# Kernel optimization log

Hardware: AMD Instinct MI355X
Metric: run time of the kernel (lower is better)

## Reference

```python
import jax, jax.numpy as jnp
import numpy as np

N, H, S, R, T = 32768, 512, 8, 64, 12

def setup_inputs() -> dict:
    key = jax.random.key(0)
    ks = jax.random.split(key, 7)
    scale = 1.0 / np.sqrt(H)
    return {
        "encodings": jax.random.normal(ks[0], (N, H), dtype=jnp.float32),
        "domain_encs": jax.random.normal(ks[1], (S, H), dtype=jnp.float32),
        "Us": jax.random.normal(ks[2], (S, H, R), dtype=jnp.float32) * scale,
        "W1": jax.random.normal(ks[3], (S, H, H), dtype=jnp.float32) * scale,
        "b1": jax.random.normal(ks[4], (S, H), dtype=jnp.float32) * 0.01,
        "W2": jax.random.normal(ks[5], (S, H, T), dtype=jnp.float32) * scale,
        "b2": jax.random.normal(ks[6], (S, T), dtype=jnp.float32) * 0.01,
    }

def reference(encodings, domain_encs, Us, W1, b1, W2, b2):
    # Mahalanobis soft routing. Original computes (p-mu) @ (U U^T) @ (p-mu)^T
    # and takes sqrt(diag) -- algebraically identical to project-then-square-sum.
    diff = encodings[None, :, :] - domain_encs[:, None, :]        # [S, N, H]
    proj = jnp.einsum('snh,shr->snr', diff, Us)                   # [S, N, R]
    dist = jnp.sqrt(jnp.sum(proj * proj, axis=-1))                # [S, N]
    alphas = jax.nn.softmax(-dist, axis=0)                        # softmax over sources

    # Per-source classifier: Dropout(eval=identity) -> ReLU -> Linear(H,H)
    # -> Dropout -> ReLU -> Linear(H,T) -> Sigmoid
    h0 = jax.nn.relu(encodings)                                   # [N, H]
    h1 = jax.nn.relu(jnp.einsum('nh,shk->snk', h0, W1) + b1[:, None, :])  # [S, N, H]
    out = jax.nn.sigmoid(jnp.einsum('snk,skt->snt', h1, W2) + b2[:, None, :])  # [S, N, T]

    # Softmax-weighted combine of expert outputs
    return jnp.sum(alphas[:, :, None] * out, axis=0)              # [N, T]
```

## Files before the change

kernel.cpp:

```cpp
#include <hip/hip_runtime.h>
#include <hip/hip_bf16.h>

typedef unsigned short u16;
typedef __bf16 bf16x8 __attribute__((ext_vector_type(8)));
typedef float f32x4 __attribute__((ext_vector_type(4)));

#define NROWS 32768
#define H 512
#define NS 8
#define NR 64
#define NT 12

#define WS_W1T   0
#define WS_UCT   4194304
#define WS_W2T   4718592
#define WS_CVEC  4849664
#define WS_DIST  4851712

union BFU { __bf16 h; u16 u; };
__device__ __forceinline__ u16 f2bf(float v) { BFU b; b.h = (__bf16)v; return b.u; }

__device__ __forceinline__ void gload16(const u16* g, u16* l) {
  __builtin_amdgcn_global_load_lds(
      (const __attribute__((address_space(1))) unsigned int*)g,
      (__attribute__((address_space(3))) unsigned int*)l, 16, 0, 0);
}

__global__ __launch_bounds__(256) void prep(
    const float* __restrict__ W1, u16* __restrict__ W1T,
    const float* __restrict__ Us, u16* __restrict__ UcatT,
    const float* __restrict__ W2, u16* __restrict__ W2T,
    const float* __restrict__ mu, float* __restrict__ cvec) {
  __shared__ float tile[32][33];
  const int bid = blockIdx.x;
  const int tx = threadIdx.x, ty = threadIdx.y;
  if (bid < 2432) {
    const float* in; u16* out; int Rr, Cc, Cpad, b, r0, c0;
    if (bid < 2048) {
      in = W1; out = W1T; Rr = 512; Cc = 512; Cpad = 512;
      r0 = (bid & 15) * 32; c0 = ((bid >> 4) & 15) * 32; b = bid >> 8;
    } else if (bid < 2304) {
      int t2 = bid - 2048; in = Us; out = UcatT; Rr = 512; Cc = 64; Cpad = 64;
      r0 = (t2 & 15) * 32; c0 = ((t2 >> 4) & 1) * 32; b = t2 >> 5;
    } else {
      int t2 = bid - 2304; in = W2; out = W2T; Rr = 512; Cc = 12; Cpad = 16;
      r0 = (t2 & 15) * 32; c0 = 0; b = t2 >> 4;
    }
#pragma unroll
    for (int i = 0; i < 4; i++) {
      int r = r0 + ty + i * 8, c = c0 + tx;
      float v = 0.f;
      if (r < Rr && c < Cc) v = in[((size_t)b * Rr + r) * Cc + c];
      tile[ty + i * 8][tx] = v;
    }
    __syncthreads();
#pragma unroll
    for (int i = 0; i < 4; i++) {
      int c = c0 + ty + i * 8, r = r0 + tx;
      if (c < Cpad && r < Rr) out[((size_t)b * Cpad + c) * Rr + r] = f2bf(tile[tx][ty + i * 8]);
    }
  } else {
    const int tid = ty * 32 + tx;
    const int idx = (bid - 2432) * 4 + (tid >> 6);
    const int s = idx >> 6, r = idx & 63, t = tid & 63;
    float acc = 0.f;
#pragma unroll
    for (int k = t; k < H; k += 64) acc += mu[s * H + k] * Us[((size_t)s * H + k) * NR + r];
#pragma unroll
    for (int m = 32; m; m >>= 1) acc += __shfl_xor(acc, m, 64);
    if (t == 0) cvec[idx] = acc;
  }
}

__device__ __forceinline__ void stageW16(const u16* __restrict__ g, u16* l, int tid) {
#pragma unroll
  for (int i = 0; i < 4; i++) {
    int flat = tid + i * 256;
    int r = flat >> 5, u = flat & 31;
    gload16(g + (size_t)r * 512 + (u ^ (r & 7)) * 8, l + flat * 8);
  }
}

__device__ __forceinline__ const u16* rchunk(const u16* U, int rcol0, int q) {
  return U + ((size_t)(rcol0 + (q >> 2) * 64 + ((q >> 1) & 1) * 32)) * 512 + (q & 1) * 256;
}

__global__ __launch_bounds__(256, 2) void routing(
    const float* __restrict__ enc, const u16* __restrict__ UcatT,
    const float* __restrict__ cvec, float* __restrict__ distT) {
  __shared__ __align__(16) u16 Wst[3][32 * 256];
  __shared__ float cvS[256];

  const int tid = threadIdx.x;
  const int wave = tid >> 6, lane = tid & 63;
  const int lnm = lane & 15, lnq = lane >> 4;
  const int rb = blockIdx.x >> 1, sg = blockIdx.x & 1;
  const int row0 = rb * 128, sbase = sg * 4;
  const int rcol0 = sbase * 64;

  cvS[tid] = cvec[rcol0 + tid];

  bf16x8 efrag[2][16];
#pragma unroll
  for (int t = 0; t < 2; t++) {
    const float* rp = enc + (size_t)(row0 + wave * 32 + t * 16 + lnm) * H + lnq * 8;
#pragma unroll
    for (int ks = 0; ks < 16; ks++) {
      float4 x0 = *(const float4*)(rp + ks * 32);
      float4 x1 = *(const float4*)(rp + ks * 32 + 4);
      bf16x8 a;
      a[0] = (__bf16)x0.x; a[1] = (__bf16)x0.y; a[2] = (__bf16)x0.z; a[3] = (__bf16)x0.w;
      a[4] = (__bf16)x1.x; a[5] = (__bf16)x1.y; a[6] = (__bf16)x1.z; a[7] = (__bf16)x1.w;
      efrag[t][ks] = a;
    }
  }

  __syncthreads();

  stageW16(rchunk(UcatT, rcol0, 0), Wst[0], tid);
  int cb = 0;
  f32x4 acc[2][2];
#pragma unroll 1
  for (int j = 0; j < 4; j++) {
    float dsq[2] = {0.f, 0.f};
#pragma unroll 1
    for (int wc = 0; wc < 2; wc++) {
#pragma unroll
      for (int t = 0; t < 2; t++) { acc[t][0] = (f32x4){0,0,0,0}; acc[t][1] = (f32x4){0,0,0,0}; }
#pragma unroll
      for (int kh = 0; kh < 2; kh++) {
        const int q = j * 4 + wc * 2 + kh;
        const int nb = (cb == 2) ? 0 : cb + 1;
        if (q + 1 < 16) {
          stageW16(rchunk(UcatT, rcol0, q + 1), Wst[nb], tid);
          asm volatile("s_waitcnt vmcnt(4)" ::: "memory");
        } else {
          asm volatile("s_waitcnt vmcnt(0)" ::: "memory");
        }
        __builtin_amdgcn_s_barrier();
        const u16* buf = Wst[cb];
#pragma unroll
        for (int ks = 0; ks < 8; ks++) {
          const int uu = ((ks * 4 + lnq) ^ (lnm & 7)) * 8;
          bf16x8 w0 = *(const bf16x8*)&buf[lnm * 256 + uu];
          bf16x8 w1 = *(const bf16x8*)&buf[(16 + lnm) * 256 + uu];
#pragma unroll
          for (int t = 0; t < 2; t++) {
            acc[t][0] = __builtin_amdgcn_mfma_f32_16x16x32_bf16(w0, efrag[t][kh * 8 + ks], acc[t][0], 0, 0, 0);
            acc[t][1] = __builtin_amdgcn_mfma_f32_16x16x32_bf16(w1, efrag[t][kh * 8 + ks], acc[t][1], 0, 0, 0);
          }
        }
        cb = nb;
      }
#pragma unroll
      for (int ct = 0; ct < 2; ct++) {
        float4 cv4 = *(const float4*)&cvS[j * 64 + wc * 32 + ct * 16 + lnq * 4];
#pragma unroll
        for (int t = 0; t < 2; t++) {
          float d0 = acc[t][ct][0] - cv4.x, d1 = acc[t][ct][1] - cv4.y;
          float d2 = acc[t][ct][2] - cv4.z, d3 = acc[t][ct][3] - cv4.w;
          dsq[t] += d0 * d0 + d1 * d1 + d2 * d2 + d3 * d3;
        }
      }
    }
#pragma unroll
    for (int t = 0; t < 2; t++) {
      dsq[t] += __shfl_xor(dsq[t], 16, 64);
      dsq[t] += __shfl_xor(dsq[t], 32, 64);
    }
    if (lnq == 0) {
#pragma unroll
      for (int t = 0; t < 2; t++)
        distT[(size_t)(sbase + j) * NROWS + row0 + wave * 32 + t * 16 + lnm] = sqrtf(dsq[t]);
    }
  }
}

#define H1STR 40

__device__ __forceinline__ const u16* chunk_base(const u16* W1g, int q) {
  return W1g + ((size_t)(q >> 5) * 512 + ((q >> 1) & 15) * 32) * 512 + (q & 1) * 256;
}

__global__ __launch_bounds__(256, 2) void moe_main(
    const float* __restrict__ enc, const u16* __restrict__ W1T,
    const u16* __restrict__ W2T, const float* __restrict__ distT,
    const float* __restrict__ b1g, const float* __restrict__ b2g,
    float* __restrict__ out) {
  __shared__ __align__(16) u16 Wst[3][32 * 256];
  __shared__ __align__(16) u16 h1c[128 * H1STR];
  __shared__ float alphS[4][128];

  const int tid = threadIdx.x;
  const int wave = tid >> 6, lane = tid & 63;
  const int lnm = lane & 15, lnq = lane >> 4;
  const int rb = blockIdx.x >> 1, sg = blockIdx.x & 1;
  const int row0 = rb * 128, sbase = sg * 4;

  if (tid < 128) {
    float dv[NS], e[NS];
#pragma unroll
    for (int s2 = 0; s2 < NS; s2++) dv[s2] = distT[(size_t)s2 * NROWS + row0 + tid];
    float dmin = dv[0];
#pragma unroll
    for (int s2 = 1; s2 < NS; s2++) dmin = fminf(dmin, dv[s2]);
    float den = 0.f;
#pragma unroll
    for (int s2 = 0; s2 < NS; s2++) { e[s2] = __expf(dmin - dv[s2]); den += e[s2]; }
    float inv = 1.f / den;
#pragma unroll
    for (int jj = 0; jj < 4; jj++) alphS[jj][tid] = e[sbase + jj] * inv;
  }

  float b2v[4];
#pragma unroll
  for (int j = 0; j < 4; j++) b2v[j] = (lnm < NT) ? b2g[(sbase + j) * NT + lnm] : 0.f;

  bf16x8 efrag[2][16];
#pragma unroll
  for (int t = 0; t < 2; t++) {
    const float* rp = enc + (size_t)(row0 + wave * 32 + t * 16 + lnm) * H + lnq * 8;
#pragma unroll
    for (int ks = 0; ks < 16; ks++) {
      float4 x0 = *(const float4*)(rp + ks * 32);
      float4 x1 = *(const float4*)(rp + ks * 32 + 4);
      bf16x8 a;
      a[0] = (__bf16)fmaxf(x0.x, 0.f); a[1] = (__bf16)fmaxf(x0.y, 0.f);
      a[2] = (__bf16)fmaxf(x0.z, 0.f); a[3] = (__bf16)fmaxf(x0.w, 0.f);
      a[4] = (__bf16)fmaxf(x1.x, 0.f); a[5] = (__bf16)fmaxf(x1.y, 0.f);
      a[6] = (__bf16)fmaxf(x1.z, 0.f); a[7] = (__bf16)fmaxf(x1.w, 0.f);
      efrag[t][ks] = a;
    }
  }

  __syncthreads();

  const u16* W1g = W1T + (size_t)sbase * 512 * 512;
  stageW16(chunk_base(W1g, 0), Wst[0], tid);
  int cb = 0;
  f32x4 acc[2][2];
  float fin[2][4] = {};
#pragma unroll 1
  for (int j = 0; j < 4; j++) {
    const int s = sbase + j;
    f32x4 oacc[2] = {};
#pragma unroll 1
    for (int wc = 0; wc < 16; wc++) {
      const int q = j * 32 + wc * 2;
      float4 bq0 = *(const float4*)&b1g[s * H + wc * 32 + lnq * 4];
      float4 bq1 = *(const float4*)&b1g[s * H + wc * 32 + 16 + lnq * 4];
      bf16x8 bw = *(const bf16x8*)&W2T[((size_t)s * 16 + lnm) * H + wc * 32 + lnq * 8];
      asm volatile("" ::: "memory");
      {
        const int nb = (cb == 2) ? 0 : cb + 1;
        stageW16(chunk_base(W1g, q + 1), Wst[nb], tid);
        asm volatile("s_waitcnt vmcnt(7)" ::: "memory");
        __builtin_amdgcn_s_barrier();
        const u16* buf = Wst[cb];
#pragma unroll
        for (int t = 0; t < 2; t++) {
          acc[t][0] = (f32x4){bq0.x, bq0.y, bq0.z, bq0.w};
          acc[t][1] = (f32x4){bq1.x, bq1.y, bq1.z, bq1.w};
        }
#pragma unroll
        for (int ks = 0; ks < 8; ks++) {
          const int uu = ((ks * 4 + lnq) ^ (lnm & 7)) * 8;
          bf16x8 w0 = *(const bf16x8*)&buf[lnm * 256 + uu];
          bf16x8 w1 = *(const bf16x8*)&buf[(16 + lnm) * 256 + uu];
#pragma unroll
          for (int t = 0; t < 2; t++) {
            acc[t][0] = __builtin_amdgcn_mfma_f32_16x16x32_bf16(w0, efrag[t][ks], acc[t][0], 0, 0, 0);
            acc[t][1] = __builtin_amdgcn_mfma_f32_16x16x32_bf16(w1, efrag[t][ks], acc[t][1], 0, 0, 0);
          }
        }
        cb = nb;
      }
      {
        const int nb = (cb == 2) ? 0 : cb + 1;
        if (q + 2 < 128) {
          stageW16(chunk_base(W1g, q + 2), Wst[nb], tid);
          asm volatile("s_waitcnt vmcnt(4)" ::: "memory");
        } else {
          asm volatile("s_waitcnt vmcnt(0)" ::: "memory");
        }
        __builtin_amdgcn_s_barrier();
        const u16* buf = Wst[cb];
#pragma unroll
        for (int ks = 0; ks < 8; ks++) {
          const int uu = ((ks * 4 + lnq) ^ (lnm & 7)) * 8;
          bf16x8 w0 = *(const bf16x8*)&buf[lnm * 256 + uu];
          bf16x8 w1 = *(const bf16x8*)&buf[(16 + lnm) * 256 + uu];
#pragma unroll
          for (int t = 0; t < 2; t++) {
            acc[t][0] = __builtin_amdgcn_mfma_f32_16x16x32_bf16(w0, efrag[t][8 + ks], acc[t][0], 0, 0, 0);
            acc[t][1] = __builtin_amdgcn_mfma_f32_16x16x32_bf16(w1, efrag[t][8 + ks], acc[t][1], 0, 0, 0);
          }
        }
        cb = nb;
      }
#pragma unroll
      for (int ct = 0; ct < 2; ct++) {
#pragma unroll
        for (int t = 0; t < 2; t++) {
          union { u16 u[4]; uint2 v; } pk;
          pk.u[0] = f2bf(fmaxf(acc[t][ct][0], 0.f));
          pk.u[1] = f2bf(fmaxf(acc[t][ct][1], 0.f));
          pk.u[2] = f2bf(fmaxf(acc[t][ct][2], 0.f));
          pk.u[3] = f2bf(fmaxf(acc[t][ct][3], 0.f));
          *(uint2*)&h1c[(wave * 32 + t * 16 + lnm) * H1STR + ct * 16 + lnq * 4] = pk.v;
        }
      }
      {
#pragma unroll
        for (int t = 0; t < 2; t++) {
          bf16x8 a2 = *(const bf16x8*)&h1c[(wave * 32 + t * 16 + lnm) * H1STR + lnq * 8];
          oacc[t] = __builtin_amdgcn_mfma_f32_16x16x32_bf16(a2, bw, oacc[t], 0, 0, 0);
        }
      }
    }
    {
#pragma unroll
      for (int t = 0; t < 2; t++) {
#pragma unroll
        for (int g = 0; g < 4; g++) {
          float sig = 1.f / (1.f + __expf(-(oacc[t][g] + b2v[j])));
          fin[t][g] += alphS[j][wave * 32 + t * 16 + lnq * 4 + g] * sig;
        }
      }
    }
  }
  if (lnm < NT) {
#pragma unroll
    for (int t = 0; t < 2; t++) {
#pragma unroll
      for (int g = 0; g < 4; g++) {
        int rg = row0 + wave * 32 + t * 16 + lnq * 4 + g;
        atomicAdd(&out[(size_t)rg * NT + lnm], fin[t][g]);
      }
    }
  }
}

extern "C" void kernel_launch(void* const* d_in, const int* in_sizes, int n_in,
                              void* d_out, int out_size, void* d_ws, size_t ws_size,
                              hipStream_t stream) {
  const float* enc = (const float*)d_in[0];
  const float* mu  = (const float*)d_in[1];
  const float* Us  = (const float*)d_in[2];
  const float* W1  = (const float*)d_in[3];
  const float* b1  = (const float*)d_in[4];
  const float* W2  = (const float*)d_in[5];
  const float* b2  = (const float*)d_in[6];
  float* out = (float*)d_out;
  char* ws = (char*)d_ws;
  u16* W1T    = (u16*)(ws + WS_W1T);
  u16* UcatT  = (u16*)(ws + WS_UCT);
  u16* W2T    = (u16*)(ws + WS_W2T);
  float* cvec = (float*)(ws + WS_CVEC);
  float* distT = (float*)(ws + WS_DIST);

  prep<<<2560, dim3(32, 8, 1), 0, stream>>>(W1, W1T, Us, UcatT, W2, W2T, mu, cvec);
  routing<<<512, 256, 0, stream>>>(enc, UcatT, cvec, distT);
  hipMemsetAsync(out, 0, (size_t)out_size * sizeof(float), stream);
  moe_main<<<512, 256, 0, stream>>>(enc, W1T, W2T, distT, b1, b2, out);
}
```

Baseline: 268.3 us.

## Overlap W1 transpose and output zeroing with routing kernel blocks

The large W1 transpose-to-bf16 moves out of the prep kernel into extra blocks of the routing kernel, so it runs alongside the routing GEMM instead of before it. The output memset is replaced by zeroing blocks in that same launch, which removes a separate API call. The aim is to cut serialized launches and let the memory-bound transpose share the GPU with the compute-bound routing work. The cost is that routing_w1 now carries the routing kernel's shared memory footprint and launch bounds for the transpose blocks too, which may limit how many of them fit at once.

```diff
diff --git a/kernel.cpp b/kernel.cpp
--- a/kernel.cpp
+++ b/kernel.cpp
@@ -26,42 +26,38 @@
       (__attribute__((address_space(3))) unsigned int*)l, 16, 0, 0);
 }
 
-__global__ __launch_bounds__(256) void prep(
-    const float* __restrict__ W1, u16* __restrict__ W1T,
+__device__ __forceinline__ void tile_transpose(const float* __restrict__ in,
+    u16* __restrict__ out, int Rr, int Cc, int Cpad, int b, int r0, int c0, int tid) {
+  __shared__ float tile[32][33];
+  const int tx = tid & 31, ty = tid >> 5;
+#pragma unroll
+  for (int i = 0; i < 4; i++) {
+    int r = r0 + ty + i * 8, c = c0 + tx;
+    float v = 0.f;
+    if (r < Rr && c < Cc) v = in[((size_t)b * Rr + r) * Cc + c];
+    tile[ty + i * 8][tx] = v;
+  }
+  __syncthreads();
+#pragma unroll
+  for (int i = 0; i < 4; i++) {
+    int c = c0 + ty + i * 8, r = r0 + tx;
+    if (c < Cpad && r < Rr) out[((size_t)b * Cpad + c) * Rr + r] = f2bf(tile[tx][ty + i * 8]);
+  }
+}
+
+__global__ __launch_bounds__(256) void prepA(
     const float* __restrict__ Us, u16* __restrict__ UcatT,
     const float* __restrict__ W2, u16* __restrict__ W2T,
     const float* __restrict__ mu, float* __restrict__ cvec) {
-  __shared__ float tile[32][33];
-  const int bid = blockIdx.x;
-  const int tx = threadIdx.x, ty = threadIdx.y;
-  if (bid < 2432) {
-    const float* in; u16* out; int Rr, Cc, Cpad, b, r0, c0;
-    if (bid < 2048) {
-      in = W1; out = W1T; Rr = 512; Cc = 512; Cpad = 512;
-      r0 = (bid & 15) * 32; c0 = ((bid >> 4) & 15) * 32; b = bid >> 8;
-    } else if (bid < 2304) {
-      int t2 = bid - 2048; in = Us; out = UcatT; Rr = 512; Cc = 64; Cpad = 64;
-      r0 = (t2 & 15) * 32; c0 = ((t2 >> 4) & 1) * 32; b = t2 >> 5;
-    } else {
-      int t2 = bid - 2304; in = W2; out = W2T; Rr = 512; Cc = 12; Cpad = 16;
-      r0 = (t2 & 15) * 32; c0 = 0; b = t2 >> 4;
-    }
-#pragma unroll
-    for (int i = 0; i < 4; i++) {
-      int r = r0 + ty + i * 8, c = c0 + tx;
-      float v = 0.f;
-      if (r < Rr && c < Cc) v = in[((size_t)b * Rr + r) * Cc + c];
-      tile[ty + i * 8][tx] = v;
-    }
-    __syncthreads();
-#pragma unroll
-    for (int i = 0; i < 4; i++) {
-      int c = c0 + ty + i * 8, r = r0 + tx;
-      if (c < Cpad && r < Rr) out[((size_t)b * Cpad + c) * Rr + r] = f2bf(tile[tx][ty + i * 8]);
-    }
+  const int bid = blockIdx.x, tid = threadIdx.x;
+  if (bid < 256) {
+    tile_transpose(Us, UcatT, 512, 64, 64, bid >> 5, (bid & 15) * 32,
+                   ((bid >> 4) & 1) * 32, tid);
+  } else if (bid < 384) {
+    int t2 = bid - 256;
+    tile_transpose(W2, W2T, 512, 12, 16, t2 >> 4, (t2 & 15) * 32, 0, tid);
   } else {
-    const int tid = ty * 32 + tx;
-    const int idx = (bid - 2432) * 4 + (tid >> 6);
+    const int idx = (bid - 384) * 4 + (tid >> 6);
     const int s = idx >> 6, r = idx & 63, t = tid & 63;
     float acc = 0.f;
 #pragma unroll
@@ -85,16 +81,30 @@
   return U + ((size_t)(rcol0 + (q >> 2) * 64 + ((q >> 1) & 1) * 32)) * 512 + (q & 1) * 256;
 }
 
-__global__ __launch_bounds__(256, 2) void routing(
+__global__ __launch_bounds__(256, 2) void routing_w1(
     const float* __restrict__ enc, const u16* __restrict__ UcatT,
-    const float* __restrict__ cvec, float* __restrict__ distT) {
+    const float* __restrict__ cvec, float* __restrict__ distT,
+    const float* __restrict__ W1, u16* __restrict__ W1T,
+    float* __restrict__ out, int out_elems) {
+  const int bid = blockIdx.x, tid = threadIdx.x;
+  if (bid >= 512) {
+    if (bid < 2560) {
+      int t2 = bid - 512;
+      tile_transpose(W1, W1T, 512, 512, 512, t2 >> 8, (t2 & 15) * 32,
+                     ((t2 >> 4) & 15) * 32, tid);
+    } else {
+      int idx = ((bid - 2560) * 256 + tid) * 4;
+      if (idx < out_elems) *(float4*)&out[idx] = (float4){0.f, 0.f, 0.f, 0.f};
+    }
+    return;
+  }
+
   __shared__ __align__(16) u16 Wst[3][32 * 256];
   __shared__ float cvS[256];
 
-  const int tid = threadIdx.x;
   const int wave = tid >> 6, lane = tid & 63;
   const int lnm = lane & 15, lnq = lane >> 4;
-  const int rb = blockIdx.x >> 1, sg = blockIdx.x & 1;
+  const int rb = bid >> 1, sg = bid & 1;
   const int row0 = rb * 128, sbase = sg * 4;
   const int rcol0 = sbase * 64;
 
@@ -359,8 +369,7 @@
   float* cvec = (float*)(ws + WS_CVEC);
   float* distT = (float*)(ws + WS_DIST);
 
-  prep<<<2560, dim3(32, 8, 1), 0, stream>>>(W1, W1T, Us, UcatT, W2, W2T, mu, cvec);
-  routing<<<512, 256, 0, stream>>>(enc, UcatT, cvec, distT);
-  hipMemsetAsync(out, 0, (size_t)out_size * sizeof(float), stream);
+  prepA<<<512, 256, 0, stream>>>(Us, UcatT, W2, W2T, mu, cvec);
+  routing_w1<<<2944, 256, 0, stream>>>(enc, UcatT, cvec, distT, W1, W1T, out, out_size);
   moe_main<<<512, 256, 0, stream>>>(enc, W1T, W2T, distT, b1, b2, out);
 }
```

Measured after the change: 274.0 us. +2.1%, slower.
